# Kernel optimization log

Measured on AMD Instinct MI355X. Metric: run time of the kernel, lower is better.

Reference implementation:

```python
import jax, jax.numpy as jnp
import numpy as np

N_NODES = 50000
N_RAND_EDGES = 800000
D_FEAT = 96
K = 3
ALP = 1.0
LAM = 1.0


def setup_inputs() -> dict:
    key = jax.random.key(0)
    k1, k2, k3 = jax.random.split(key, 3)
    # random edges plus one self-loop per node (DGL-style graph with self-loops,
    # since the module computes degs = in_degrees - 1)
    src_r = jax.random.randint(k1, (N_RAND_EDGES,), 0, N_NODES, dtype=jnp.int32)
    dst_r = jax.random.randint(k2, (N_RAND_EDGES,), 0, N_NODES, dtype=jnp.int32)
    loops = jnp.arange(N_NODES, dtype=jnp.int32)
    src = jnp.concatenate([src_r, loops])
    dst = jnp.concatenate([dst_r, loops])
    features = jax.random.normal(k3, (N_NODES, D_FEAT), dtype=jnp.float32)
    return {"src": src, "dst": dst, "features": features}


def reference(src, dst, features):
    n = features.shape[0]
    # in-degrees of the self-loop graph; degs excludes the self-loop
    in_deg = jax.ops.segment_sum(jnp.ones_like(dst, dtype=features.dtype), dst,
                                 num_segments=n)
    degs = in_deg - 1.0
    norm_lambd_1 = (LAM * degs + 1.0) ** -1.0       # [N]
    norm05 = jnp.sqrt(degs + 1.0)                    # [N]
    norm_05 = (degs + 1.0) ** -0.5                   # [N]
    norm_lambd_1 = norm_lambd_1[:, None]
    norm05 = norm05[:, None]
    norm_05 = norm_05[:, None]

    h = features
    h_pre = h
    h_initial = h * norm_lambd_1
    for _ in range(K):
        h = h * norm_05
        # copy_u / sum: aggregate source features into destinations
        h = jax.ops.segment_sum(h[src], dst, num_segments=n)
        h = h * norm_lambd_1 * norm05
        h = ALP * LAM * h + (1.0 - ALP) * h_pre + ALP * h_initial
        h_pre = h
    return h
```

## Files before the change

kernel.cpp:

```cpp
#include <hip/hip_runtime.h>

#define NDF 96
#define NCHB 12
#define BSH 8
#define BCAP 8192
#define TILE 4096

typedef unsigned short u16x8 __attribute__((ext_vector_type(8)));

__device__ __forceinline__ float bf2f(unsigned short u) {
    union { unsigned int i; float f; } x;
    x.i = ((unsigned int)u) << 16;
    return x.f;
}
__device__ __forceinline__ unsigned short f2bf(float f) {
    union { float f; unsigned int i; } x;
    x.f = f;
    unsigned int i = x.i;
    return (unsigned short)((i + 0x7FFFu + ((i >> 16) & 1u)) >> 16);
}


__global__ void k_binit(int* __restrict__ bcount) {
    bcount[threadIdx.x] = 0;
}

__global__ void __launch_bounds__(512) k_passA(
        const int* __restrict__ src, const int* __restrict__ dst, int nr,
        int* __restrict__ bcount, unsigned int* __restrict__ bucket) {
    __shared__ unsigned int stage[TILE];
    __shared__ int cnt[256], sstart[256], lcur[256], gbase[256];
    __shared__ int wsum4[4], pref4[4];
    int tid  = threadIdx.x;
    int tile = blockIdx.x * TILE;
    int cnt_e = min(TILE, nr - tile);
    if (tid < 256) cnt[tid] = 0;
    __syncthreads();
    for (int k = tid; k < cnt_e; k += 512)
        atomicAdd(&cnt[dst[tile + k] >> BSH], 1);
    __syncthreads();
    int x = 0, val = 0;
    if (tid < 256) {
        x = cnt[tid];
        val = x;
        int lane = tid & 63;
        #pragma unroll
        for (int off = 1; off < 64; off <<= 1) {
            int t = __shfl_up(val, off, 64);
            if (lane >= off) val += t;
        }
        if (lane == 63) wsum4[tid >> 6] = val;
    }
    __syncthreads();
    if (tid == 0) {
        int s = 0;
        #pragma unroll
        for (int w = 0; w < 4; ++w) { pref4[w] = s; s += wsum4[w]; }
    }
    __syncthreads();
    if (tid < 256) {
        sstart[tid] = val + pref4[tid >> 6] - x;
        lcur[tid]   = 0;
        gbase[tid]  = (x > 0) ? atomicAdd(&bcount[tid], x) : 0;
    }
    __syncthreads();
    for (int k = tid; k < cnt_e; k += 512) {
        int d = dst[tile + k];
        int s = src[tile + k];
        int b = d >> BSH;
        int pos = atomicAdd(&lcur[b], 1);
        stage[sstart[b] + pos] = ((unsigned int)d << 16) | (unsigned int)s;
    }
    __syncthreads();
    for (int k = tid; k < cnt_e; k += 512) {
        unsigned int u = stage[k];
        int b = (int)(u >> 24);
        bucket[((size_t)b << 13) + gbase[b] + (k - sstart[b])] = u;
    }
}

__global__ void __launch_bounds__(256) k_passB(
        const int* __restrict__ bcount, const unsigned int* __restrict__ bucket,
        int* __restrict__ rdeg, int n) {
    __shared__ int dl[256];
    int tid = threadIdx.x;
    int b   = blockIdx.x;
    dl[tid] = 0;
    __syncthreads();
    int cb = bcount[b];
    const unsigned int* __restrict__ bp = bucket + ((size_t)b << 13);
    for (int k = tid; k < cb; k += 256)
        atomicAdd(&dl[(bp[k] >> 16) & 255], 1);
    __syncthreads();
    int node = (b << BSH) + tid;
    if (node < n) rdeg[node] = dl[tid];
}

__global__ void __launch_bounds__(1024) k_scan_blk(const int* __restrict__ rdeg, int n,
                                                   int* __restrict__ row_ptr,
                                                   int* __restrict__ blk_sums) {
    __shared__ int wsum[16];
    int tid  = threadIdx.x;
    int lane = tid & 63;
    int wid  = tid >> 6;
    int i = blockIdx.x * 1024 + tid;
    int x = (i < n) ? rdeg[i] : 0;
    int val = x;
    #pragma unroll
    for (int off = 1; off < 64; off <<= 1) {
        int t = __shfl_up(val, off, 64);
        if (lane >= off) val += t;
    }
    if (lane == 63) wsum[wid] = val;
    __syncthreads();
    if (wid == 0) {
        int w = (lane < 16) ? wsum[lane] : 0;
        #pragma unroll
        for (int off = 1; off < 16; off <<= 1) {
            int t = __shfl_up(w, off, 64);
            if (lane >= off) w += t;
        }
        if (lane < 16) wsum[lane] = w;
    }
    __syncthreads();
    int wave_off = (wid > 0) ? wsum[wid - 1] : 0;
    if (i < n) row_ptr[i] = val + wave_off - x;
    if (tid == 0) blk_sums[blockIdx.x] = wsum[15];
}

__global__ void __launch_bounds__(64) k_scan_top(const int* __restrict__ blk_sums,
                                                 int* __restrict__ blk_off, int nblk) {
    int lane = threadIdx.x;
    int carry = 0;
    for (int base = 0; base < nblk; base += 64) {
        int i = base + lane;
        int x = (i < nblk) ? blk_sums[i] : 0;
        int val = x;
        #pragma unroll
        for (int off = 1; off < 64; off <<= 1) {
            int t = __shfl_up(val, off, 64);
            if (lane >= off) val += t;
        }
        if (i < nblk) blk_off[i] = carry + val - x;
        carry += __shfl(val, 63, 64);
    }
}

__global__ void __launch_bounds__(512) k_passC(
        const int* __restrict__ bcount, const unsigned int* __restrict__ bucket,
        const int* __restrict__ row_ptr, const int* __restrict__ blk_off,
        unsigned short* __restrict__ csr, int n, int nr) {
    __shared__ int cur[257];
    __shared__ unsigned short stg[BCAP];
    int tid = threadIdx.x;
    int b   = blockIdx.x;
    if (tid <= 256) {
        int node = (b << BSH) + tid;
        cur[tid] = (node >= n) ? nr : (row_ptr[node] + blk_off[node >> 10]);
    }
    __syncthreads();
    int base  = cur[0];
    int total = cur[256] - base;
    __syncthreads();
    if (tid < 256) cur[tid] -= base;
    __syncthreads();
    int cb = bcount[b];
    const unsigned int* __restrict__ bp = bucket + ((size_t)b << 13);
    for (int k = tid; k < cb; k += 512) {
        unsigned int u = bp[k];
        int p = atomicAdd(&cur[(u >> 16) & 255], 1);
        stg[p] = (unsigned short)(u & 0xFFFFu);
    }
    __syncthreads();
    for (int k = tid; k < total; k += 512)
        csr[base + k] = stg[k];
}


__global__ void __launch_bounds__(256) k_scale(
        const float* __restrict__ feat, const int* __restrict__ rdeg,
        unsigned short* __restrict__ hs, unsigned short* __restrict__ hinit,
        int nt ) {
    int t = blockIdx.x * blockDim.x + threadIdx.x;
    if (t >= nt) return;
    int v = t / NCHB;
    float d  = (float)(rdeg[v] + 1);
    float s  = rsqrtf(d);
    float iv = 1.0f / d;
    const float4* f4 = (const float4*)feat;
    float4 fa = f4[t * 2];
    float4 fb = f4[t * 2 + 1];
    u16x8 o, oi;
    o[0] = f2bf(fa.x * s);  oi[0] = f2bf(fa.x * iv);
    o[1] = f2bf(fa.y * s);  oi[1] = f2bf(fa.y * iv);
    o[2] = f2bf(fa.z * s);  oi[2] = f2bf(fa.z * iv);
    o[3] = f2bf(fa.w * s);  oi[3] = f2bf(fa.w * iv);
    o[4] = f2bf(fb.x * s);  oi[4] = f2bf(fb.x * iv);
    o[5] = f2bf(fb.y * s);  oi[5] = f2bf(fb.y * iv);
    o[6] = f2bf(fb.z * s);  oi[6] = f2bf(fb.z * iv);
    o[7] = f2bf(fb.w * s);  oi[7] = f2bf(fb.w * iv);
    ((u16x8*)hs)[t]    = o;
    ((u16x8*)hinit)[t] = oi;
}

template <int LAST>
__global__ void __launch_bounds__(256) k_prop(
        const unsigned short* __restrict__ hs, const int* __restrict__ row_ptr,
        const int* __restrict__ blk_off, const unsigned short* __restrict__ csr_src,
        const int* __restrict__ rdeg, const unsigned short* __restrict__ hinit,
        void* __restrict__ outp, int n, int nr, int nt) {
    int t = blockIdx.x * blockDim.x + threadIdx.x;
    if (t >= nt) return;
    int v = t / NCHB;
    int c = t - v * NCHB;
    int beg = row_ptr[v] + blk_off[v >> 10];
    int end = (v + 1 == n) ? nr : (row_ptr[v + 1] + blk_off[(v + 1) >> 10]);
    const u16x8* __restrict__ hs8 = (const u16x8*)hs;
    u16x8 own = hs8[t];
    float a0 = bf2f(own[0]), a1 = bf2f(own[1]);
    float a2 = bf2f(own[2]), a3 = bf2f(own[3]);
    float a4 = bf2f(own[4]), a5 = bf2f(own[5]);
    float a6 = bf2f(own[6]), a7 = bf2f(own[7]);

    #define ACC(HV) do { \
        a0 += bf2f((HV)[0]); a1 += bf2f((HV)[1]); \
        a2 += bf2f((HV)[2]); a3 += bf2f((HV)[3]); \
        a4 += bf2f((HV)[4]); a5 += bf2f((HV)[5]); \
        a6 += bf2f((HV)[6]); a7 += bf2f((HV)[7]); } while (0)

    int j = beg;
    while (j + 8 <= end) {
        int s0 = (int)csr_src[j    ], s1 = (int)csr_src[j + 1];
        int s2 = (int)csr_src[j + 2], s3 = (int)csr_src[j + 3];
        int s4 = (int)csr_src[j + 4], s5 = (int)csr_src[j + 5];
        int s6 = (int)csr_src[j + 6], s7 = (int)csr_src[j + 7];
        u16x8 h0 = hs8[s0 * NCHB + c];
        u16x8 h1 = hs8[s1 * NCHB + c];
        u16x8 h2 = hs8[s2 * NCHB + c];
        u16x8 h3 = hs8[s3 * NCHB + c];
        u16x8 h4 = hs8[s4 * NCHB + c];
        u16x8 h5 = hs8[s5 * NCHB + c];
        u16x8 h6 = hs8[s6 * NCHB + c];
        u16x8 h7 = hs8[s7 * NCHB + c];
        ACC(h0); ACC(h1); ACC(h2); ACC(h3);
        ACC(h4); ACC(h5); ACC(h6); ACC(h7);
        j += 8;
    }
    if (j + 4 <= end) {
        int s0 = (int)csr_src[j    ], s1 = (int)csr_src[j + 1];
        int s2 = (int)csr_src[j + 2], s3 = (int)csr_src[j + 3];
        u16x8 h0 = hs8[s0 * NCHB + c];
        u16x8 h1 = hs8[s1 * NCHB + c];
        u16x8 h2 = hs8[s2 * NCHB + c];
        u16x8 h3 = hs8[s3 * NCHB + c];
        ACC(h0); ACC(h1); ACC(h2); ACC(h3);
        j += 4;
    }
    if (j + 2 <= end) {
        int s0 = (int)csr_src[j], s1 = (int)csr_src[j + 1];
        u16x8 h0 = hs8[s0 * NCHB + c];
        u16x8 h1 = hs8[s1 * NCHB + c];
        ACC(h0); ACC(h1);
        j += 2;
    }
    if (j < end) {
        int s0 = (int)csr_src[j];
        u16x8 h0 = hs8[s0 * NCHB + c];
        ACC(h0);
    }
    #undef ACC

    float sv = rsqrtf((float)(rdeg[v] + 1));
    u16x8 hi = ((const u16x8*)hinit)[t];
    float r0 = a0 * sv + bf2f(hi[0]);
    float r1 = a1 * sv + bf2f(hi[1]);
    float r2 = a2 * sv + bf2f(hi[2]);
    float r3 = a3 * sv + bf2f(hi[3]);
    float r4 = a4 * sv + bf2f(hi[4]);
    float r5 = a5 * sv + bf2f(hi[5]);
    float r6 = a6 * sv + bf2f(hi[6]);
    float r7 = a7 * sv + bf2f(hi[7]);
    if (LAST) {
        float4* o4 = (float4*)outp;
        o4[t * 2]     = make_float4(r0, r1, r2, r3);
        o4[t * 2 + 1] = make_float4(r4, r5, r6, r7);
    } else {
        u16x8 o;
        o[0] = f2bf(r0 * sv); o[1] = f2bf(r1 * sv);
        o[2] = f2bf(r2 * sv); o[3] = f2bf(r3 * sv);
        o[4] = f2bf(r4 * sv); o[5] = f2bf(r5 * sv);
        o[6] = f2bf(r6 * sv); o[7] = f2bf(r7 * sv);
        ((u16x8*)outp)[t] = o;
    }
}


extern "C" void kernel_launch(void* const* d_in, const int* in_sizes, int n_in,
                              void* d_out, int out_size, void* d_ws, size_t ws_size,
                              hipStream_t stream) {
    const int*   src  = (const int*)d_in[0];
    const int*   dst  = (const int*)d_in[1];
    const float* feat = (const float*)d_in[2];
    const int E  = in_sizes[0];
    const int n  = in_sizes[2] / NDF;
    const int nr = E - n;
    float* out = (float*)d_out;

    char* p = (char*)d_ws;
    auto take = [&](size_t bytes) {
        char* r = p;
        p += (bytes + 255) & ~size_t(255);
        return r;
    };
    const int nblk = (n + 1023) / 1024;
    const int NBK  = (n + 255) >> 8;
    int* bcount        = (int*)take(256 * 4);
    int* blk_sums      = (int*)take((size_t)nblk * 4);
    int* blk_off       = (int*)take((size_t)nblk * 4);
    int* row_ptr       = (int*)take((size_t)(n + 1) * 4);
    int* rdeg          = (int*)take((size_t)n * 4);
    unsigned int* bucket = (unsigned int*)take((size_t)256 * BCAP * 4);
    unsigned short* csr  = (unsigned short*)take((size_t)nr * 2);
    unsigned short* hsA   = (unsigned short*)take((size_t)n * NDF * 2);
    unsigned short* hsB   = (unsigned short*)take((size_t)n * NDF * 2);
    unsigned short* hinit = (unsigned short*)take((size_t)n * NDF * 2);
    (void)ws_size;

    const int nt = n * NCHB;
    const int bT = (nt + 255) / 256;
    const int bA = (nr + TILE - 1) / TILE;

    k_binit   <<<1, 256, 0, stream>>>(bcount);
    k_passA   <<<bA, 512, 0, stream>>>(src, dst, nr, bcount, bucket);
    k_passB   <<<NBK, 256, 0, stream>>>(bcount, bucket, rdeg, n);
    k_scan_blk<<<nblk, 1024, 0, stream>>>(rdeg, n, row_ptr, blk_sums);
    k_scan_top<<<1, 64, 0, stream>>>(blk_sums, blk_off, nblk);
    k_passC   <<<NBK, 512, 0, stream>>>(bcount, bucket, row_ptr, blk_off, csr, n, nr);

    k_scale<<<bT, 256, 0, stream>>>(feat, rdeg, hsA, hinit, nt);

    k_prop<0><<<bT, 256, 0, stream>>>(hsA, row_ptr, blk_off, csr, rdeg, hinit, hsB, n, nr, nt);
    k_prop<0><<<bT, 256, 0, stream>>>(hsB, row_ptr, blk_off, csr, rdeg, hinit, hsA, n, nr, nt);
    k_prop<1><<<bT, 256, 0, stream>>>(hsA, row_ptr, blk_off, csr, rdeg, hinit, out, n, nr, nt);
}
```

Before: 119.9 us.

## Fuse CSR build, scan and scaling into one per-bucket kernel with padded rows

Merges the degree count, the two global scan kernels, the CSR fill and the feature scaling into a single per-bucket kernel. It does this by giving each 256-node bucket a fixed CSR slab and padding every row to a multiple of 8 with a dummy node index n, whose feature row is zeroed. The propagation kernel then reads neighbour indices as aligned 8-wide vectors with no tail handling. This removes four launches and the cross-block scan. In exchange it adds wasted gathers on the padding, a larger CSR buffer, and assumes each bucket fits in BCAP after padding.

```diff
diff --git a/kernel.cpp b/kernel.cpp
--- a/kernel.cpp
+++ b/kernel.cpp
@@ -20,9 +20,13 @@
     return (unsigned short)((i + 0x7FFFu + ((i >> 16) & 1u)) >> 16);
 }
 
-
-__global__ void k_binit(int* __restrict__ bcount) {
-    bcount[threadIdx.x] = 0;
+__global__ void k_binit(int* __restrict__ bcount, unsigned short* __restrict__ hsA,
+                        unsigned short* __restrict__ hsB, int n) {
+    int t = threadIdx.x;
+    bcount[t] = 0;
+    u16x8 z = {0, 0, 0, 0, 0, 0, 0, 0};
+    if (t < NCHB)            ((u16x8*)hsA)[(size_t)n * NCHB + t]        = z;
+    else if (t < 2 * NCHB)   ((u16x8*)hsB)[(size_t)n * NCHB + (t - NCHB)] = z;
 }
 
 __global__ void __launch_bounds__(512) k_passA(
@@ -79,143 +83,109 @@
     }
 }
 
-__global__ void __launch_bounds__(256) k_passB(
+__global__ void __launch_bounds__(512) k_passBC(
         const int* __restrict__ bcount, const unsigned int* __restrict__ bucket,
-        int* __restrict__ rdeg, int n) {
-    __shared__ int dl[256];
+        const float* __restrict__ feat, int* __restrict__ rdeg_g,
+        int* __restrict__ row_ptr, unsigned short* __restrict__ csr,
+        unsigned short* __restrict__ hs, unsigned short* __restrict__ hinit,
+        int n) {
+    __shared__ int dl[256], cur[256];
+    __shared__ int wsum4[4], pref4[4];
+    __shared__ int total_s;
+    __shared__ unsigned short stg[BCAP];
     int tid = threadIdx.x;
     int b   = blockIdx.x;
-    dl[tid] = 0;
+    if (tid < 256) dl[tid] = 0;
     __syncthreads();
     int cb = bcount[b];
     const unsigned int* __restrict__ bp = bucket + ((size_t)b << 13);
-    for (int k = tid; k < cb; k += 256)
+    for (int k = tid; k < cb; k += 512)
         atomicAdd(&dl[(bp[k] >> 16) & 255], 1);
     __syncthreads();
-    int node = (b << BSH) + tid;
-    if (node < n) rdeg[node] = dl[tid];
-}
-
-__global__ void __launch_bounds__(1024) k_scan_blk(const int* __restrict__ rdeg, int n,
-                                                   int* __restrict__ row_ptr,
-                                                   int* __restrict__ blk_sums) {
-    __shared__ int wsum[16];
-    int tid  = threadIdx.x;
-    int lane = tid & 63;
-    int wid  = tid >> 6;
-    int i = blockIdx.x * 1024 + tid;
-    int x = (i < n) ? rdeg[i] : 0;
-    int val = x;
-    #pragma unroll
-    for (int off = 1; off < 64; off <<= 1) {
-        int t = __shfl_up(val, off, 64);
-        if (lane >= off) val += t;
-    }
-    if (lane == 63) wsum[wid] = val;
-    __syncthreads();
-    if (wid == 0) {
-        int w = (lane < 16) ? wsum[lane] : 0;
-        #pragma unroll
-        for (int off = 1; off < 16; off <<= 1) {
-            int t = __shfl_up(w, off, 64);
-            if (lane >= off) w += t;
-        }
-        if (lane < 16) wsum[lane] = w;
-    }
-    __syncthreads();
-    int wave_off = (wid > 0) ? wsum[wid - 1] : 0;
-    if (i < n) row_ptr[i] = val + wave_off - x;
-    if (tid == 0) blk_sums[blockIdx.x] = wsum[15];
-}
-
-__global__ void __launch_bounds__(64) k_scan_top(const int* __restrict__ blk_sums,
-                                                 int* __restrict__ blk_off, int nblk) {
-    int lane = threadIdx.x;
-    int carry = 0;
-    for (int base = 0; base < nblk; base += 64) {
-        int i = base + lane;
-        int x = (i < nblk) ? blk_sums[i] : 0;
-        int val = x;
+    int x = 0, val = 0;
+    if (tid < 256) {
+        x = (dl[tid] + 7) & ~7;
+        val = x;
+        int lane = tid & 63;
         #pragma unroll
         for (int off = 1; off < 64; off <<= 1) {
             int t = __shfl_up(val, off, 64);
             if (lane >= off) val += t;
         }
-        if (i < nblk) blk_off[i] = carry + val - x;
-        carry += __shfl(val, 63, 64);
-    }
-}
-
-__global__ void __launch_bounds__(512) k_passC(
-        const int* __restrict__ bcount, const unsigned int* __restrict__ bucket,
-        const int* __restrict__ row_ptr, const int* __restrict__ blk_off,
-        unsigned short* __restrict__ csr, int n, int nr) {
-    __shared__ int cur[257];
-    __shared__ unsigned short stg[BCAP];
-    int tid = threadIdx.x;
-    int b   = blockIdx.x;
-    if (tid <= 256) {
+        if (lane == 63) wsum4[tid >> 6] = val;
+    }
+    __syncthreads();
+    if (tid == 0) {
+        int s = 0;
+        #pragma unroll
+        for (int w = 0; w < 4; ++w) { pref4[w] = s; s += wsum4[w]; }
+        total_s = s;
+    }
+    __syncthreads();
+    if (tid < 256) {
+        int off_ex = val + pref4[tid >> 6] - x;
+        cur[tid] = off_ex;
         int node = (b << BSH) + tid;
-        cur[tid] = (node >= n) ? nr : (row_ptr[node] + blk_off[node >> 10]);
-    }
-    __syncthreads();
-    int base  = cur[0];
-    int total = cur[256] - base;
-    __syncthreads();
-    if (tid < 256) cur[tid] -= base;
-    __syncthreads();
-    int cb = bcount[b];
-    const unsigned int* __restrict__ bp = bucket + ((size_t)b << 13);
+        if (node < n) {
+            rdeg_g[node]  = dl[tid];
+            row_ptr[node] = (b << 13) + off_ex;
+        }
+    }
+    __syncthreads();
+    int total = total_s;
+    for (int k = tid; k < total; k += 512)
+        stg[k] = (unsigned short)n;
+    __syncthreads();
     for (int k = tid; k < cb; k += 512) {
         unsigned int u = bp[k];
         int p = atomicAdd(&cur[(u >> 16) & 255], 1);
         stg[p] = (unsigned short)(u & 0xFFFFu);
     }
     __syncthreads();
+    unsigned short* __restrict__ cout = csr + ((size_t)b << 13);
     for (int k = tid; k < total; k += 512)
-        csr[base + k] = stg[k];
-}
-
-
-__global__ void __launch_bounds__(256) k_scale(
-        const float* __restrict__ feat, const int* __restrict__ rdeg,
-        unsigned short* __restrict__ hs, unsigned short* __restrict__ hinit,
-        int nt ) {
-    int t = blockIdx.x * blockDim.x + threadIdx.x;
-    if (t >= nt) return;
-    int v = t / NCHB;
-    float d  = (float)(rdeg[v] + 1);
-    float s  = rsqrtf(d);
-    float iv = 1.0f / d;
-    const float4* f4 = (const float4*)feat;
-    float4 fa = f4[t * 2];
-    float4 fb = f4[t * 2 + 1];
-    u16x8 o, oi;
-    o[0] = f2bf(fa.x * s);  oi[0] = f2bf(fa.x * iv);
-    o[1] = f2bf(fa.y * s);  oi[1] = f2bf(fa.y * iv);
-    o[2] = f2bf(fa.z * s);  oi[2] = f2bf(fa.z * iv);
-    o[3] = f2bf(fa.w * s);  oi[3] = f2bf(fa.w * iv);
-    o[4] = f2bf(fb.x * s);  oi[4] = f2bf(fb.x * iv);
-    o[5] = f2bf(fb.y * s);  oi[5] = f2bf(fb.y * iv);
-    o[6] = f2bf(fb.z * s);  oi[6] = f2bf(fb.z * iv);
-    o[7] = f2bf(fb.w * s);  oi[7] = f2bf(fb.w * iv);
-    ((u16x8*)hs)[t]    = o;
-    ((u16x8*)hinit)[t] = oi;
+        cout[k] = stg[k];
+    const float4* __restrict__ f4 = (const float4*)feat;
+    for (int k = tid; k < 256 * NCHB; k += 512) {
+        int lv = k / NCHB;
+        int c  = k - lv * NCHB;
+        int v  = (b << BSH) + lv;
+        if (v >= n) break;
+        float d  = (float)(dl[lv] + 1);
+        float s  = rsqrtf(d);
+        float iv = 1.0f / d;
+        int ci = v * NCHB + c;
+        float4 fa = f4[(size_t)ci * 2];
+        float4 fb = f4[(size_t)ci * 2 + 1];
+        u16x8 o, oi;
+        o[0] = f2bf(fa.x * s);  oi[0] = f2bf(fa.x * iv);
+        o[1] = f2bf(fa.y * s);  oi[1] = f2bf(fa.y * iv);
+        o[2] = f2bf(fa.z * s);  oi[2] = f2bf(fa.z * iv);
+        o[3] = f2bf(fa.w * s);  oi[3] = f2bf(fa.w * iv);
+        o[4] = f2bf(fb.x * s);  oi[4] = f2bf(fb.x * iv);
+        o[5] = f2bf(fb.y * s);  oi[5] = f2bf(fb.y * iv);
+        o[6] = f2bf(fb.z * s);  oi[6] = f2bf(fb.z * iv);
+        o[7] = f2bf(fb.w * s);  oi[7] = f2bf(fb.w * iv);
+        ((u16x8*)hs)[ci]    = o;
+        ((u16x8*)hinit)[ci] = oi;
+    }
 }
 
 template <int LAST>
 __global__ void __launch_bounds__(256) k_prop(
         const unsigned short* __restrict__ hs, const int* __restrict__ row_ptr,
-        const int* __restrict__ blk_off, const unsigned short* __restrict__ csr_src,
-        const int* __restrict__ rdeg, const unsigned short* __restrict__ hinit,
-        void* __restrict__ outp, int n, int nr, int nt) {
+        const int* __restrict__ rdeg, const unsigned short* __restrict__ csr,
+        const unsigned short* __restrict__ hinit,
+        void* __restrict__ outp, int nt) {
     int t = blockIdx.x * blockDim.x + threadIdx.x;
     if (t >= nt) return;
     int v = t / NCHB;
     int c = t - v * NCHB;
-    int beg = row_ptr[v] + blk_off[v >> 10];
-    int end = (v + 1 == n) ? nr : (row_ptr[v + 1] + blk_off[(v + 1) >> 10]);
-    const u16x8* __restrict__ hs8 = (const u16x8*)hs;
+    int beg = row_ptr[v];
+    int dv  = rdeg[v];
+    int nit = (dv + 7) >> 3;
+    const u16x8* __restrict__ hs8  = (const u16x8*)hs;
+    const u16x8* __restrict__ csr8 = (const u16x8*)csr + (beg >> 3);
     u16x8 own = hs8[t];
     float a0 = bf2f(own[0]), a1 = bf2f(own[1]);
     float a2 = bf2f(own[2]), a3 = bf2f(own[3]);
@@ -228,49 +198,22 @@
         a4 += bf2f((HV)[4]); a5 += bf2f((HV)[5]); \
         a6 += bf2f((HV)[6]); a7 += bf2f((HV)[7]); } while (0)
 
-    int j = beg;
-    while (j + 8 <= end) {
-        int s0 = (int)csr_src[j    ], s1 = (int)csr_src[j + 1];
-        int s2 = (int)csr_src[j + 2], s3 = (int)csr_src[j + 3];
-        int s4 = (int)csr_src[j + 4], s5 = (int)csr_src[j + 5];
-        int s6 = (int)csr_src[j + 6], s7 = (int)csr_src[j + 7];
-        u16x8 h0 = hs8[s0 * NCHB + c];
-        u16x8 h1 = hs8[s1 * NCHB + c];
-        u16x8 h2 = hs8[s2 * NCHB + c];
-        u16x8 h3 = hs8[s3 * NCHB + c];
-        u16x8 h4 = hs8[s4 * NCHB + c];
-        u16x8 h5 = hs8[s5 * NCHB + c];
-        u16x8 h6 = hs8[s6 * NCHB + c];
-        u16x8 h7 = hs8[s7 * NCHB + c];
+    for (int it = 0; it < nit; ++it) {
+        u16x8 sv8 = csr8[it];
+        u16x8 h0 = hs8[(int)sv8[0] * NCHB + c];
+        u16x8 h1 = hs8[(int)sv8[1] * NCHB + c];
+        u16x8 h2 = hs8[(int)sv8[2] * NCHB + c];
+        u16x8 h3 = hs8[(int)sv8[3] * NCHB + c];
+        u16x8 h4 = hs8[(int)sv8[4] * NCHB + c];
+        u16x8 h5 = hs8[(int)sv8[5] * NCHB + c];
+        u16x8 h6 = hs8[(int)sv8[6] * NCHB + c];
+        u16x8 h7 = hs8[(int)sv8[7] * NCHB + c];
         ACC(h0); ACC(h1); ACC(h2); ACC(h3);
         ACC(h4); ACC(h5); ACC(h6); ACC(h7);
-        j += 8;
-    }
-    if (j + 4 <= end) {
-        int s0 = (int)csr_src[j    ], s1 = (int)csr_src[j + 1];
-        int s2 = (int)csr_src[j + 2], s3 = (int)csr_src[j + 3];
-        u16x8 h0 = hs8[s0 * NCHB + c];
-        u16x8 h1 = hs8[s1 * NCHB + c];
-        u16x8 h2 = hs8[s2 * NCHB + c];
-        u16x8 h3 = hs8[s3 * NCHB + c];
-        ACC(h0); ACC(h1); ACC(h2); ACC(h3);
-        j += 4;
-    }
-    if (j + 2 <= end) {
-        int s0 = (int)csr_src[j], s1 = (int)csr_src[j + 1];
-        u16x8 h0 = hs8[s0 * NCHB + c];
-        u16x8 h1 = hs8[s1 * NCHB + c];
-        ACC(h0); ACC(h1);
-        j += 2;
-    }
-    if (j < end) {
-        int s0 = (int)csr_src[j];
-        u16x8 h0 = hs8[s0 * NCHB + c];
-        ACC(h0);
     }
     #undef ACC
 
-    float sv = rsqrtf((float)(rdeg[v] + 1));
+    float sv = rsqrtf((float)(dv + 1));
     u16x8 hi = ((const u16x8*)hinit)[t];
     float r0 = a0 * sv + bf2f(hi[0]);
     float r1 = a1 * sv + bf2f(hi[1]);
@@ -312,17 +255,14 @@
         p += (bytes + 255) & ~size_t(255);
         return r;
     };
-    const int nblk = (n + 1023) / 1024;
-    const int NBK  = (n + 255) >> 8;
-    int* bcount        = (int*)take(256 * 4);
-    int* blk_sums      = (int*)take((size_t)nblk * 4);
-    int* blk_off       = (int*)take((size_t)nblk * 4);
-    int* row_ptr       = (int*)take((size_t)(n + 1) * 4);
-    int* rdeg          = (int*)take((size_t)n * 4);
+    const int NBK = (n + 255) >> 8;
+    int* bcount          = (int*)take(256 * 4);
+    int* row_ptr         = (int*)take((size_t)n * 4);
+    int* rdeg            = (int*)take((size_t)n * 4);
     unsigned int* bucket = (unsigned int*)take((size_t)256 * BCAP * 4);
-    unsigned short* csr  = (unsigned short*)take((size_t)nr * 2);
-    unsigned short* hsA   = (unsigned short*)take((size_t)n * NDF * 2);
-    unsigned short* hsB   = (unsigned short*)take((size_t)n * NDF * 2);
+    unsigned short* csr  = (unsigned short*)take((size_t)256 * BCAP * 2);
+    unsigned short* hsA   = (unsigned short*)take((size_t)(n + 1) * NDF * 2);
+    unsigned short* hsB   = (unsigned short*)take((size_t)(n + 1) * NDF * 2);
     unsigned short* hinit = (unsigned short*)take((size_t)n * NDF * 2);
     (void)ws_size;
 
@@ -330,16 +270,12 @@
     const int bT = (nt + 255) / 256;
     const int bA = (nr + TILE - 1) / TILE;
 
-    k_binit   <<<1, 256, 0, stream>>>(bcount);
-    k_passA   <<<bA, 512, 0, stream>>>(src, dst, nr, bcount, bucket);
-    k_passB   <<<NBK, 256, 0, stream>>>(bcount, bucket, rdeg, n);
-    k_scan_blk<<<nblk, 1024, 0, stream>>>(rdeg, n, row_ptr, blk_sums);
-    k_scan_top<<<1, 64, 0, stream>>>(blk_sums, blk_off, nblk);
-    k_passC   <<<NBK, 512, 0, stream>>>(bcount, bucket, row_ptr, blk_off, csr, n, nr);
-
-    k_scale<<<bT, 256, 0, stream>>>(feat, rdeg, hsA, hinit, nt);
-
-    k_prop<0><<<bT, 256, 0, stream>>>(hsA, row_ptr, blk_off, csr, rdeg, hinit, hsB, n, nr, nt);
-    k_prop<0><<<bT, 256, 0, stream>>>(hsB, row_ptr, blk_off, csr, rdeg, hinit, hsA, n, nr, nt);
-    k_prop<1><<<bT, 256, 0, stream>>>(hsA, row_ptr, blk_off, csr, rdeg, hinit, out, n, nr, nt);
-}
+    k_binit <<<1, 256, 0, stream>>>(bcount, hsA, hsB, n);
+    k_passA <<<bA, 512, 0, stream>>>(src, dst, nr, bcount, bucket);
+    k_passBC<<<NBK, 512, 0, stream>>>(bcount, bucket, feat, rdeg, row_ptr,
+                                      csr, hsA, hinit, n);
+
+    k_prop<0><<<bT, 256, 0, stream>>>(hsA, row_ptr, rdeg, csr, hinit, hsB, nt);
+    k_prop<0><<<bT, 256, 0, stream>>>(hsB, row_ptr, rdeg, csr, hinit, hsA, nt);
+    k_prop<1><<<bT, 256, 0, stream>>>(hsA, row_ptr, rdeg, csr, hinit, out, nt);
+}
```

Result: faster. 109.5 us (-8.6%).
